# Optimization experiments

Hardware: AMD Instinct MI355X
Metric: run time of the kernel (lower is better)

## Reference

```python
import jax, jax.numpy as jnp
import numpy as np

TEMPERATURE = 0.07
NEG_INF = -1e9  # fp16-safe large negative for masking


def setup_inputs() -> dict:
    key = jax.random.key(0)
    k1, k2 = jax.random.split(key)
    N, D = 4096, 1024
    logits1 = jax.random.normal(k1, (N, D), dtype=jnp.float32)
    logits2 = jax.random.normal(k2, (N, D), dtype=jnp.float32)
    return {"logits1": logits1, "logits2": logits2}


def reference(logits1, logits2):
    # L2-normalize each view along feature dim
    z1 = logits1 / jnp.linalg.norm(logits1, axis=1, keepdims=True)
    z2 = logits2 / jnp.linalg.norm(logits2, axis=1, keepdims=True)
    z = jnp.concatenate([z1, z2], axis=0)  # [2N, D]
    N2 = z.shape[0]
    N = N2 // 2
    sim = jnp.matmul(z, z.T) / TEMPERATURE  # [2N, 2N]
    # positive pair index: i <-> i+N (mod 2N)
    pos_idx = jnp.concatenate([jnp.arange(N) + N, jnp.arange(N)])
    pos_vals = sim[jnp.arange(N2), pos_idx]  # [2N]
    # CE over row = [pos, negs(excl self & pos)] with label 0 is equivalent to
    # -pos + logsumexp over all columns except the diagonal (pos counted once).
    diag_mask = jnp.eye(N2, dtype=bool)
    sim_masked = jnp.where(diag_mask, NEG_INF, sim)
    lse = jax.nn.logsumexp(sim_masked, axis=1)  # [2N]
    loss = jnp.mean(lse - pos_vals)
    return loss
```

## Files before the change

kernel.cpp:

```cpp
#include <hip/hip_runtime.h>
#include <hip/hip_bf16.h>


#define NPAIR 4096
#define NROWS 8192
#define DIM   1024
#define NOFF  496
#define NTAIL 96
#define NKT   16
#define INV_T 14.285714285714286f

typedef __attribute__((ext_vector_type(4))) float f32x4;
typedef __attribute__((ext_vector_type(2))) long  i64x2;

#define GLOAD_LDS16(g, l)                                              \
  __builtin_amdgcn_global_load_lds(                                    \
      (const __attribute__((address_space(1))) void*)(g),              \
      (__attribute__((address_space(3))) void*)(l), 16, 0, 0)

#define MFMA_FP8(A, B, C)                                              \
  __builtin_amdgcn_mfma_f32_16x16x32_fp8_fp8((long)(A), (long)(B), (C), 0, 0, 0)

#define WAIT_VM(N)  asm volatile("s_waitcnt vmcnt(" #N ")" ::: "memory")
#define BARRIER()   { __builtin_amdgcn_s_barrier();                    \
                      __builtin_amdgcn_sched_barrier(0); }

__global__ __launch_bounds__(256) void normalize_kernel(
    const float* __restrict__ l1, const float* __restrict__ l2,
    unsigned char* __restrict__ Z, float* __restrict__ pos,
    float* __restrict__ rowsum) {
  const int i = blockIdx.x;
  const int t = threadIdx.x;
  if (t < 2) rowsum[i * 2 + t] = 0.f;
  const float4 a = ((const float4*)(l1 + (size_t)i * DIM))[t];
  const float4 b = ((const float4*)(l2 + (size_t)i * DIM))[t];
  float s1 = a.x*a.x + a.y*a.y + a.z*a.z + a.w*a.w;
  float s2 = b.x*b.x + b.y*b.y + b.z*b.z + b.w*b.w;
  float d  = a.x*b.x + a.y*b.y + a.z*b.z + a.w*b.w;

  #pragma unroll
  for (int off = 32; off; off >>= 1) {
    s1 += __shfl_down(s1, off);
    s2 += __shfl_down(s2, off);
    d  += __shfl_down(d,  off);
  }
  __shared__ float red[3][4];
  __shared__ float fin[3];
  const int wave = t >> 6, lane = t & 63;
  if (lane == 0) { red[0][wave] = s1; red[1][wave] = s2; red[2][wave] = d; }
  __syncthreads();
  if (t == 0) {
    float S1 = red[0][0] + red[0][1] + red[0][2] + red[0][3];
    float S2 = red[1][0] + red[1][1] + red[1][2] + red[1][3];
    float DD = red[2][0] + red[2][1] + red[2][2] + red[2][3];
    float r1 = rsqrtf(S1), r2 = rsqrtf(S2);
    fin[0] = r1; fin[1] = r2;
    pos[i] = DD * r1 * r2 * INV_T;
  }
  __syncthreads();
  const float r1 = fin[0], r2 = fin[1];
  int pa = __builtin_amdgcn_cvt_pk_fp8_f32(a.x * r1, a.y * r1, 0, false);
  pa     = __builtin_amdgcn_cvt_pk_fp8_f32(a.z * r1, a.w * r1, pa, true);
  int pb = __builtin_amdgcn_cvt_pk_fp8_f32(b.x * r2, b.y * r2, 0, false);
  pb     = __builtin_amdgcn_cvt_pk_fp8_f32(b.z * r2, b.w * r2, pb, true);
  const int k0 = t * 4;
  const int noff = (k0 >> 6) * 64 + (((k0 >> 3) & 3) << 4)
                 + (((k0 >> 5) & 1) << 3) + (k0 & 7);
  *(int*)(Z + (size_t)i * DIM + noff) = pa;
  *(int*)(Z + (size_t)(i + NPAIR) * DIM + noff) = pb;
}

__global__ __launch_bounds__(512, 2) void ntxent_gemm_all(
    const unsigned char* __restrict__ Z, float* __restrict__ rowsum) {
  __shared__ unsigned char lds[131072];

  const int t    = threadIdx.x;
  const int wid  = t >> 6;
  const int lane = t & 63;
  const int lrow = lane & 15;
  const int kgrp = lane >> 4;

  if (blockIdx.x < NOFF) {
    const int wm = wid >> 2;
    const int wn = wid & 3;

    const int idx = (blockIdx.x & 7) * 62 + (blockIdx.x >> 3);
    int bj = (int)((1.0f + sqrtf(1.0f + 8.0f * (float)idx)) * 0.5f);
    while (bj * (bj - 1) / 2 > idx) --bj;
    while ((bj + 1) * bj / 2 <= idx) ++bj;
    const int bi = idx - bj * (bj - 1) / 2;
    const int brow = bi * 256, bcol = bj * 256;

    auto stage_tile = [&](int kt, int bufoff) {
      #pragma unroll
      for (int op = 0; op < 2; ++op) {
        const int rowbase = op ? bcol : brow;
        const int opoff   = op ? 16384 : 0;
        #pragma unroll
        for (int i = 0; i < 2; ++i) {
          const int cb = wid * 128 + i * 64;
          const int c  = cb + lane;
          const int r  = c >> 2;
          const int lc = (c & 3) ^ ((r >> 1) & 3);
          GLOAD_LDS16(Z + (size_t)(rowbase + r) * DIM + kt * 64 + lc * 16,
                      lds + bufoff + opoff + cb * 16);
        }
      }
    };
    auto ld16 = [&](int bufoff, int opoff, int row) -> i64x2 {
      return *(const i64x2*)(lds + bufoff + opoff + row * 64
                             + ((kgrp ^ ((row >> 1) & 3)) << 4));
    };

    i64x2 pa[8], pb[4], qa[8], qb[4];
    f32x4 acc[8][4];
    #pragma unroll
    for (int i = 0; i < 8; ++i)
      #pragma unroll
      for (int j = 0; j < 4; ++j) acc[i][j] = (f32x4){0.f, 0.f, 0.f, 0.f};

#define READF(A_, B_, BO)                                              \
  { _Pragma("unroll") for (int mi = 0; mi < 8; ++mi)                   \
      A_[mi] = ld16((BO), 0, wm * 128 + mi * 16 + lrow);               \
    _Pragma("unroll") for (int ni = 0; ni < 4; ++ni)                   \
      B_[ni] = ld16((BO), 16384, wn * 64 + ni * 16 + lrow); }
#define MMF(A_, B_)                                                    \
  { __builtin_amdgcn_s_setprio(1);                                     \
    _Pragma("unroll") for (int mi = 0; mi < 8; ++mi)                   \
    _Pragma("unroll") for (int ni = 0; ni < 4; ++ni)                   \
      acc[mi][ni] = MFMA_FP8(A_[mi].x, B_[ni].x, acc[mi][ni]);         \
    _Pragma("unroll") for (int mi = 0; mi < 8; ++mi)                   \
    _Pragma("unroll") for (int ni = 0; ni < 4; ++ni)                   \
      acc[mi][ni] = MFMA_FP8(A_[mi].y, B_[ni].y, acc[mi][ni]);         \
    __builtin_amdgcn_s_setprio(0); }

    stage_tile(0, 0);
    stage_tile(1, 32768);
    stage_tile(2, 65536);
    WAIT_VM(8);
    __syncthreads();
    READF(pa, pb, 0);

    #pragma unroll
    for (int h = 0; h < NKT; ++h) {
      const int bo_next  = ((h + 1) & 3) * 32768;
      const int bo_stage = ((h + 3) & 3) * 32768;
      if (h <= NKT - 3) { WAIT_VM(4); } else { WAIT_VM(0); }
      BARRIER();
      if (h + 1 < NKT) {
        if (h & 1) { READF(pa, pb, bo_next); }
        else       { READF(qa, qb, bo_next); }
      }
      if (h + 3 < NKT) stage_tile(h + 3, bo_stage);
      if (h & 1) { MMF(qa, qb); } else { MMF(pa, pb); }
    }
#undef READF
#undef MMF

    #pragma unroll
    for (int mi = 0; mi < 8; ++mi)
      #pragma unroll
      for (int ni = 0; ni < 4; ++ni)
        #pragma unroll
        for (int j = 0; j < 4; ++j)
          acc[mi][ni][j] = __expf((acc[mi][ni][j] - 1.0f) * INV_T);
    #pragma unroll
    for (int mi = 0; mi < 8; ++mi) {
      float rs[4] = {0.f, 0.f, 0.f, 0.f};
      #pragma unroll
      for (int ni = 0; ni < 4; ++ni)
        #pragma unroll
        for (int j = 0; j < 4; ++j) rs[j] += acc[mi][ni][j];
      #pragma unroll
      for (int j = 0; j < 4; ++j) {
        float s = rs[j];
        s += __shfl_xor(s, 1);
        s += __shfl_xor(s, 2);
        s += __shfl_xor(s, 4);
        s += __shfl_xor(s, 8);
        if (lrow == 0)
          atomicAdd(&rowsum[brow + wm * 128 + mi * 16 + kgrp * 4 + j], s);
      }
    }
    #pragma unroll
    for (int ni = 0; ni < 4; ++ni) {
      float cs = 0.f;
      #pragma unroll
      for (int mi = 0; mi < 8; ++mi)
        cs += acc[mi][ni][0] + acc[mi][ni][1] + acc[mi][ni][2] + acc[mi][ni][3];
      cs += __shfl_xor(cs, 16);
      cs += __shfl_xor(cs, 32);
      if (kgrp == 0)
        atomicAdd(&rowsum[bcol + wn * 64 + ni * 16 + lrow], cs);
    }
  } else {
    const int b2 = blockIdx.x - NOFF;
    const int d  = b2 / 3, ty = b2 - d * 3;
    const int arow0 = d * 256 + (ty == 2 ? 128 : 0);
    const int bcol0 = d * 256 + (ty >= 1 ? 128 : 0);
    const int wm = wid >> 2;
    const int wn = wid & 3;

    auto stage = [&](int kt, int buf, int rowbase, int opoff) {
      const int cb = wid * 64;
      const int c  = cb + lane;
      const int r  = c >> 2;
      const int lc = (c & 3) ^ ((r >> 1) & 3);
      GLOAD_LDS16(Z + (size_t)(rowbase + r) * DIM + kt * 64 + lc * 16,
                  lds + buf * 16384 + opoff + cb * 16);
    };
    auto ld16 = [&](int buf, int opoff, int row) -> i64x2 {
      return *(const i64x2*)(lds + buf * 16384 + opoff + row * 64
                             + ((kgrp ^ ((row >> 1) & 3)) << 4));
    };

    f32x4 acc[4][2];
    #pragma unroll
    for (int i = 0; i < 4; ++i)
      #pragma unroll
      for (int j = 0; j < 2; ++j) acc[i][j] = (f32x4){0.f, 0.f, 0.f, 0.f};

    stage(0, 0, arow0, 0); stage(0, 0, bcol0, 8192);
    stage(1, 1, arow0, 0); stage(1, 1, bcol0, 8192);
    WAIT_VM(2);
    __builtin_amdgcn_s_barrier();

    int bcur = 0, bnext = 1, bfree = 2;
    for (int kt = 0; kt < NKT; ++kt) {
      i64x2 a[4], b[2];
      #pragma unroll
      for (int mi = 0; mi < 4; ++mi)
        a[mi] = ld16(bcur, 0, wm * 64 + mi * 16 + lrow);
      #pragma unroll
      for (int ni = 0; ni < 2; ++ni)
        b[ni] = ld16(bcur, 8192, wn * 32 + ni * 16 + lrow);
      if (kt + 2 < NKT) {
        stage(kt + 2, bfree, arow0, 0);
        stage(kt + 2, bfree, bcol0, 8192);
      }
      asm volatile("s_waitcnt lgkmcnt(0)" ::: "memory");
      __builtin_amdgcn_sched_barrier(0);
      __builtin_amdgcn_s_setprio(1);
      #pragma unroll
      for (int mi = 0; mi < 4; ++mi)
        #pragma unroll
        for (int ni = 0; ni < 2; ++ni)
          acc[mi][ni] = MFMA_FP8(a[mi].x, b[ni].x, acc[mi][ni]);
      #pragma unroll
      for (int mi = 0; mi < 4; ++mi)
        #pragma unroll
        for (int ni = 0; ni < 2; ++ni)
          acc[mi][ni] = MFMA_FP8(a[mi].y, b[ni].y, acc[mi][ni]);
      __builtin_amdgcn_s_setprio(0);
      if (kt + 2 < NKT) { WAIT_VM(2); }
      else if (kt + 1 < NKT) { WAIT_VM(0); }
      __builtin_amdgcn_s_barrier();
      const int tmp = bcur; bcur = bnext; bnext = bfree; bfree = tmp;
    }

    #pragma unroll
    for (int mi = 0; mi < 4; ++mi)
      #pragma unroll
      for (int ni = 0; ni < 2; ++ni) {
        const int gcol = bcol0 + wn * 32 + ni * 16 + lrow;
        #pragma unroll
        for (int j = 0; j < 4; ++j) {
          const int grow = arow0 + wm * 64 + mi * 16 + kgrp * 4 + j;
          const float v = acc[mi][ni][j];
          acc[mi][ni][j] = (gcol > grow) ? __expf((v - 1.0f) * INV_T) : 0.f;
        }
      }
    #pragma unroll
    for (int mi = 0; mi < 4; ++mi) {
      float rs[4] = {0.f, 0.f, 0.f, 0.f};
      #pragma unroll
      for (int ni = 0; ni < 2; ++ni)
        #pragma unroll
        for (int j = 0; j < 4; ++j) rs[j] += acc[mi][ni][j];
      #pragma unroll
      for (int j = 0; j < 4; ++j) {
        float s = rs[j];
        s += __shfl_xor(s, 1);
        s += __shfl_xor(s, 2);
        s += __shfl_xor(s, 4);
        s += __shfl_xor(s, 8);
        if (lrow == 0)
          atomicAdd(&rowsum[arow0 + wm * 64 + mi * 16 + kgrp * 4 + j], s);
      }
    }
    #pragma unroll
    for (int ni = 0; ni < 2; ++ni) {
      float cs = 0.f;
      #pragma unroll
      for (int mi = 0; mi < 4; ++mi)
        cs += acc[mi][ni][0] + acc[mi][ni][1] + acc[mi][ni][2] + acc[mi][ni][3];
      cs += __shfl_xor(cs, 16);
      cs += __shfl_xor(cs, 32);
      if (kgrp == 0)
        atomicAdd(&rowsum[bcol0 + wn * 32 + ni * 16 + lrow], cs);
    }
  }
}

__global__ __launch_bounds__(1024) void finalize_kernel(
    const float* __restrict__ rowsum, const float* __restrict__ pos,
    float* __restrict__ out) {
  const int t = threadIdx.x;
  float ls = 0.f, ps = 0.f;
  for (int i = t; i < NROWS; i += 1024) ls += logf(rowsum[i]);
  for (int i = t; i < NPAIR; i += 1024) ps += pos[i];
  #pragma unroll
  for (int off = 32; off; off >>= 1) {
    ls += __shfl_down(ls, off);
    ps += __shfl_down(ps, off);
  }
  __shared__ float sls[16], sps[16];
  const int wave = t >> 6, lane = t & 63;
  if (lane == 0) { sls[wave] = ls; sps[wave] = ps; }
  __syncthreads();
  if (t == 0) {
    float LS = 0.f, PS = 0.f;
    #pragma unroll
    for (int w = 0; w < 16; ++w) { LS += sls[w]; PS += sps[w]; }
    out[0] = INV_T + LS / (float)NROWS - PS / (float)NPAIR;
  }
}

extern "C" void kernel_launch(void* const* d_in, const int* in_sizes, int n_in,
                              void* d_out, int out_size, void* d_ws, size_t ws_size,
                              hipStream_t stream) {
  const float* l1 = (const float*)d_in[0];
  const float* l2 = (const float*)d_in[1];
  float* out = (float*)d_out;

  char* ws = (char*)d_ws;
  unsigned char* Z = (unsigned char*)ws;
  float* rowsum = (float*)(ws + (size_t)NROWS * DIM);
  float* pos    = rowsum + NROWS;

  normalize_kernel<<<NPAIR, 256, 0, stream>>>(l1, l2, Z, pos, rowsum);
  ntxent_gemm_all<<<NOFF + NTAIL, 512, 0, stream>>>(Z, rowsum);
  finalize_kernel<<<1, 1024, 0, stream>>>(rowsum, pos, out);
}
```

Before: 91.05 us.

## Shrink off-diagonal GEMM tiles to 256x128 with triple-buffered LDS for higher occupancy

Splits each 256x256 upper-triangle tile into 256x128 tiles, doubling the main block count, and cuts per-block LDS to three 24KB buffers so four 512-thread blocks can share a CU. Per-wave accumulators shrink from 8x4 to 4x4 MFMA tiles, which frees registers. The pipeline changes from a 4-buffer, 3-deep prefetch to a 3-buffer rotation that waits for all loads before each barrier. The aim is better CU fill and latency hiding through occupancy, at the cost of less operand reuse per block, more global traffic, more atomics, and a shallower prefetch.

New measurement: 253.9 us. +178.9%, slower.

```diff
diff --git a/kernel.cpp b/kernel.cpp
--- a/kernel.cpp
+++ b/kernel.cpp
@@ -5,7 +5,7 @@
 #define NPAIR 4096
 #define NROWS 8192
 #define DIM   1024
-#define NOFF  496
+#define NMAIN 992
 #define NTAIL 96
 #define NKT   16
 #define INV_T 14.285714285714286f
@@ -70,9 +70,9 @@
   *(int*)(Z + (size_t)(i + NPAIR) * DIM + noff) = pb;
 }
 
-__global__ __launch_bounds__(512, 2) void ntxent_gemm_all(
+__global__ __launch_bounds__(512, 4) void ntxent_gemm_all(
     const unsigned char* __restrict__ Z, float* __restrict__ rowsum) {
-  __shared__ unsigned char lds[131072];
+  __shared__ unsigned char lds[3 * 24576];
 
   const int t    = threadIdx.x;
   const int wid  = t >> 6;
@@ -80,31 +80,34 @@
   const int lrow = lane & 15;
   const int kgrp = lane >> 4;
 
-  if (blockIdx.x < NOFF) {
-    const int wm = wid >> 2;
-    const int wn = wid & 3;
-
-    const int idx = (blockIdx.x & 7) * 62 + (blockIdx.x >> 3);
-    int bj = (int)((1.0f + sqrtf(1.0f + 8.0f * (float)idx)) * 0.5f);
-    while (bj * (bj - 1) / 2 > idx) --bj;
-    while ((bj + 1) * bj / 2 <= idx) ++bj;
-    const int bi = idx - bj * (bj - 1) / 2;
-    const int brow = bi * 256, bcol = bj * 256;
+  if (blockIdx.x < NMAIN) {
+    const int wm = wid >> 1;
+    const int wn = wid & 1;
+
+    const int idx = (blockIdx.x & 7) * 124 + (blockIdx.x >> 3);
+    int bi = (int)((63.0f - sqrtf(3969.0f - 4.0f * (float)idx)) * 0.5f);
+    while ((bi + 1) * (62 - bi) <= idx) ++bi;
+    while (bi * (63 - bi) > idx) --bi;
+    const int bj = 2 * bi + 2 + (idx - bi * (63 - bi));
+    const int brow = bi * 256, bcol = bj * 128;
 
     auto stage_tile = [&](int kt, int bufoff) {
       #pragma unroll
-      for (int op = 0; op < 2; ++op) {
-        const int rowbase = op ? bcol : brow;
-        const int opoff   = op ? 16384 : 0;
-        #pragma unroll
-        for (int i = 0; i < 2; ++i) {
-          const int cb = wid * 128 + i * 64;
-          const int c  = cb + lane;
-          const int r  = c >> 2;
-          const int lc = (c & 3) ^ ((r >> 1) & 3);
-          GLOAD_LDS16(Z + (size_t)(rowbase + r) * DIM + kt * 64 + lc * 16,
-                      lds + bufoff + opoff + cb * 16);
-        }
+      for (int i = 0; i < 2; ++i) {
+        const int cb = wid * 128 + i * 64;
+        const int c  = cb + lane;
+        const int r  = c >> 2;
+        const int lc = (c & 3) ^ ((r >> 1) & 3);
+        GLOAD_LDS16(Z + (size_t)(brow + r) * DIM + kt * 64 + lc * 16,
+                    lds + bufoff + cb * 16);
+      }
+      {
+        const int cb = wid * 64;
+        const int c  = cb + lane;
+        const int r  = c >> 2;
+        const int lc = (c & 3) ^ ((r >> 1) & 3);
+        GLOAD_LDS16(Z + (size_t)(bcol + r) * DIM + kt * 64 + lc * 16,
+                    lds + bufoff + 16384 + cb * 16);
       }
     };
     auto ld16 = [&](int bufoff, int opoff, int row) -> i64x2 {
@@ -112,60 +115,62 @@
                              + ((kgrp ^ ((row >> 1) & 3)) << 4));
     };
 
-    i64x2 pa[8], pb[4], qa[8], qb[4];
-    f32x4 acc[8][4];
-    #pragma unroll
-    for (int i = 0; i < 8; ++i)
+    i64x2 pa[4], pb[4], qa[4], qb[4];
+    f32x4 acc[4][4];
+    #pragma unroll
+    for (int i = 0; i < 4; ++i)
       #pragma unroll
       for (int j = 0; j < 4; ++j) acc[i][j] = (f32x4){0.f, 0.f, 0.f, 0.f};
 
 #define READF(A_, B_, BO)                                              \
-  { _Pragma("unroll") for (int mi = 0; mi < 8; ++mi)                   \
-      A_[mi] = ld16((BO), 0, wm * 128 + mi * 16 + lrow);               \
+  { _Pragma("unroll") for (int mi = 0; mi < 4; ++mi)                   \
+      A_[mi] = ld16((BO), 0, wm * 64 + mi * 16 + lrow);                \
     _Pragma("unroll") for (int ni = 0; ni < 4; ++ni)                   \
       B_[ni] = ld16((BO), 16384, wn * 64 + ni * 16 + lrow); }
 #define MMF(A_, B_)                                                    \
   { __builtin_amdgcn_s_setprio(1);                                     \
-    _Pragma("unroll") for (int mi = 0; mi < 8; ++mi)                   \
+    _Pragma("unroll") for (int mi = 0; mi < 4; ++mi)                   \
     _Pragma("unroll") for (int ni = 0; ni < 4; ++ni)                   \
       acc[mi][ni] = MFMA_FP8(A_[mi].x, B_[ni].x, acc[mi][ni]);         \
-    _Pragma("unroll") for (int mi = 0; mi < 8; ++mi)                   \
+    _Pragma("unroll") for (int mi = 0; mi < 4; ++mi)                   \
     _Pragma("unroll") for (int ni = 0; ni < 4; ++ni)                   \
       acc[mi][ni] = MFMA_FP8(A_[mi].y, B_[ni].y, acc[mi][ni]);         \
     __builtin_amdgcn_s_setprio(0); }
 
-    stage_tile(0, 0);
-    stage_tile(1, 32768);
-    stage_tile(2, 65536);
-    WAIT_VM(8);
+    int oA = 0, oB = 24576, oC = 49152;
+    stage_tile(0, oA);
+    stage_tile(1, oB);
+    WAIT_VM(0);
     __syncthreads();
-    READF(pa, pb, 0);
-
-    #pragma unroll
-    for (int h = 0; h < NKT; ++h) {
-      const int bo_next  = ((h + 1) & 3) * 32768;
-      const int bo_stage = ((h + 3) & 3) * 32768;
-      if (h <= NKT - 3) { WAIT_VM(4); } else { WAIT_VM(0); }
+    READF(pa, pb, oA);
+
+    for (int I = 0; I < 8; ++I) {
+      const int j = 2 * I;
+      WAIT_VM(0);
       BARRIER();
-      if (h + 1 < NKT) {
-        if (h & 1) { READF(pa, pb, bo_next); }
-        else       { READF(qa, qb, bo_next); }
-      }
-      if (h + 3 < NKT) stage_tile(h + 3, bo_stage);
-      if (h & 1) { MMF(qa, qb); } else { MMF(pa, pb); }
+      READF(qa, qb, oB);
+      if (j + 2 < NKT) stage_tile(j + 2, oC);
+      MMF(pa, pb);
+      { const int tmp = oA; oA = oB; oB = oC; oC = tmp; }
+      WAIT_VM(0);
+      BARRIER();
+      if (j + 2 < NKT) READF(pa, pb, oB);
+      if (j + 3 < NKT) stage_tile(j + 3, oC);
+      MMF(qa, qb);
+      { const int tmp = oA; oA = oB; oB = oC; oC = tmp; }
     }
 #undef READF
 #undef MMF
 
     #pragma unroll
-    for (int mi = 0; mi < 8; ++mi)
+    for (int mi = 0; mi < 4; ++mi)
       #pragma unroll
       for (int ni = 0; ni < 4; ++ni)
         #pragma unroll
         for (int j = 0; j < 4; ++j)
           acc[mi][ni][j] = __expf((acc[mi][ni][j] - 1.0f) * INV_T);
     #pragma unroll
-    for (int mi = 0; mi < 8; ++mi) {
+    for (int mi = 0; mi < 4; ++mi) {
       float rs[4] = {0.f, 0.f, 0.f, 0.f};
       #pragma unroll
       for (int ni = 0; ni < 4; ++ni)
@@ -179,14 +184,14 @@
         s += __shfl_xor(s, 4);
         s += __shfl_xor(s, 8);
         if (lrow == 0)
-          atomicAdd(&rowsum[brow + wm * 128 + mi * 16 + kgrp * 4 + j], s);
+          atomicAdd(&rowsum[brow + wm * 64 + mi * 16 + kgrp * 4 + j], s);
       }
     }
     #pragma unroll
     for (int ni = 0; ni < 4; ++ni) {
       float cs = 0.f;
       #pragma unroll
-      for (int mi = 0; mi < 8; ++mi)
+      for (int mi = 0; mi < 4; ++mi)
         cs += acc[mi][ni][0] + acc[mi][ni][1] + acc[mi][ni][2] + acc[mi][ni][3];
       cs += __shfl_xor(cs, 16);
       cs += __shfl_xor(cs, 32);
@@ -194,7 +199,7 @@
         atomicAdd(&rowsum[bcol + wn * 64 + ni * 16 + lrow], cs);
     }
   } else {
-    const int b2 = blockIdx.x - NOFF;
+    const int b2 = blockIdx.x - NMAIN;
     const int d  = b2 / 3, ty = b2 - d * 3;
     const int arow0 = d * 256 + (ty == 2 ? 128 : 0);
     const int bcol0 = d * 256 + (ty >= 1 ? 128 : 0);
@@ -339,6 +344,6 @@
   float* pos    = rowsum + NROWS;
 
   normalize_kernel<<<NPAIR, 256, 0, stream>>>(l1, l2, Z, pos, rowsum);
-  ntxent_gemm_all<<<NOFF + NTAIL, 512, 0, stream>>>(Z, rowsum);
+  ntxent_gemm_all<<<NMAIN + NTAIL, 512, 0, stream>>>(Z, rowsum);
   finalize_kernel<<<1, 1024, 0, stream>>>(rowsum, pos, out);
 }
```
